# Optimization experiments

Hardware: AMD Instinct MI355X
Metric: run time of the kernel (lower is better)

The kernel has to match this reference:

```python
import jax, jax.numpy as jnp
import numpy as np

NEG_SLOPE = 0.2


def _gcn_conv(x, edge_index, W, b):
    # Standard GCNConv: y = D^-1/2 (A + I) D^-1/2 (x W) + b
    N = x.shape[0]
    loop = jnp.arange(N, dtype=edge_index.dtype)
    src = jnp.concatenate([edge_index[0], loop])  # [E+N]
    dst = jnp.concatenate([edge_index[1], loop])  # [E+N]
    deg = jax.ops.segment_sum(jnp.ones_like(dst, dtype=x.dtype), dst, num_segments=N)
    dinv = jnp.where(deg > 0, jax.lax.rsqrt(deg), 0.0)
    norm = dinv[src] * dinv[dst]                  # [E+N]
    h = x @ W                                     # [N, out] dense GEMM
    msg = h[src] * norm[:, None]                  # irregular gather, [E+N, out]
    agg = jax.ops.segment_sum(msg, dst, num_segments=N)  # irregular scatter
    return agg + b


def setup_inputs() -> dict:
    key = jax.random.key(0)
    ks = jax.random.split(key, 5)
    N, E, d_in, d_hid = 50000, 800000, 256, 512
    s = lambda fan_in, fan_out: np.sqrt(6.0 / (fan_in + fan_out))
    return {
        "x": jax.random.normal(ks[0], (N, d_in), dtype=jnp.float32),
        "edge_index": jax.random.randint(ks[1], (2, E), 0, N, dtype=jnp.int64),
        "W_gcn": jax.random.uniform(ks[2], (d_in, d_hid), jnp.float32, -s(d_in, d_hid), s(d_in, d_hid)),
        "b_gcn": jnp.zeros((d_hid,), jnp.float32),
        "W2": jax.random.uniform(ks[3], (d_hid, d_hid), jnp.float32, -s(d_hid, d_hid), s(d_hid, d_hid)),
        "b2": jnp.zeros((d_hid,), jnp.float32),
        "W_out": jax.random.uniform(ks[4], (d_hid, 1), jnp.float32, -s(d_hid, 1), s(d_hid, 1)),
        "b_out": jnp.zeros((1,), jnp.float32),
    }


def reference(x, edge_index, W_gcn, b_gcn, W2, b2, W_out, b_out):
    h = _gcn_conv(x, edge_index, W_gcn, b_gcn)           # [N, 512]
    h = jax.nn.leaky_relu(h, NEG_SLOPE)
    h = jax.nn.leaky_relu(h @ W2 + b2, NEG_SLOPE)        # [N, 512]
    return h @ W_out + b_out                             # [N, 1]
```

## Files before the change

kernel.cpp:

```cpp
#include <hip/hip_runtime.h>

#define D_IN  256
#define D_HID 512
#define NEG_SLOPE 0.2f
#define SCAN_CHUNK 2048

typedef __attribute__((ext_vector_type(8))) short short8;
typedef __attribute__((ext_vector_type(4))) float floatx4;

__device__ __forceinline__ unsigned short f2bf(float f) {
    unsigned int u = __float_as_uint(f);
    u += 0x7fffu + ((u >> 16) & 1u);
    return (unsigned short)(u >> 16);
}
__device__ __forceinline__ float bf2f(unsigned short u) {
    return __uint_as_float(((unsigned int)u) << 16);
}

__device__ __forceinline__ int eidx(const void* ei, long pos, int is64) {
    return is64 ? (int)((const long long*)ei)[pos] : ((const int*)ei)[pos];
}

__global__ __launch_bounds__(256) void k_init(const float* __restrict__ x,
                                              unsigned short* __restrict__ xb,
                                              int* __restrict__ deg, int N,
                                              const unsigned int* __restrict__ ei,
                                              int npairs, int* flag,
                                              const float* __restrict__ W_gcn,
                                              unsigned short* __restrict__ Wgt,
                                              const float* __restrict__ W2,
                                              unsigned short* __restrict__ W2t,
                                              const float* __restrict__ b_out,
                                              float* __restrict__ outacc,
                                              long xthreads) {
    long t = (long)blockIdx.x * blockDim.x + threadIdx.x;
    if (t < xthreads) {
        long i = t * 4;
        float4 v = *(const float4*)(x + i);
        ushort4 o;
        o.x = f2bf(v.x); o.y = f2bf(v.y); o.z = f2bf(v.z); o.w = f2bf(v.w);
        *(ushort4*)(xb + i) = o;
        if (t < N) deg[t] = 0;
        if (blockIdx.x == 0) {
            __shared__ int nz;
            if (threadIdx.x == 0) nz = 0;
            __syncthreads();
            for (int p = threadIdx.x; p < npairs; p += blockDim.x)
                if (ei[2 * p + 1] != 0) nz = 1;
            __syncthreads();
            if (threadIdx.x == 0) *flag = nz ? 0 : 1;
        }
        return;
    }
    long u = t - xthreads;
    if (u < (long)D_IN * D_HID) {
        int tt = (int)u;
        int n = tt / D_IN, k = tt - n * D_IN;
        Wgt[tt] = f2bf(W_gcn[(long)k * D_HID + n]);
        return;
    }
    u -= (long)D_IN * D_HID;
    if (u < (long)D_HID * D_HID) {
        int tt = (int)u;
        int n = tt / D_HID, k = tt - n * D_HID;
        W2t[tt] = f2bf(W2[(long)k * D_HID + n]);
        return;
    }
    u -= (long)D_HID * D_HID;
    if (u < N) outacc[u] = b_out[0];
}

__global__ void k_deg_count(const void* __restrict__ ei, const int* __restrict__ flag,
                            int* __restrict__ deg, int E) {
    int e = blockIdx.x * blockDim.x + threadIdx.x;
    if (e < E) atomicAdd(&deg[eidx(ei, (long)E + e, *flag)], 1);
}

__global__ __launch_bounds__(256) void k_scan1(const int* __restrict__ deg,
                                               int* __restrict__ bsum, int N) {
    int base = blockIdx.x * SCAN_CHUNK;
    int hi = min(base + SCAN_CHUNK, N);
    int s = 0;
    for (int i = base + threadIdx.x; i < hi; i += 256) s += deg[i];
#pragma unroll
    for (int off = 32; off > 0; off >>= 1) s += __shfl_down(s, off, 64);
    __shared__ int lds[4];
    if ((threadIdx.x & 63) == 0) lds[threadIdx.x >> 6] = s;
    __syncthreads();
    if (threadIdx.x == 0) bsum[blockIdx.x] = lds[0] + lds[1] + lds[2] + lds[3];
}

__global__ __launch_bounds__(256) void k_scan23(const int* __restrict__ deg,
                                                const int* __restrict__ bsum, int NB,
                                                int* __restrict__ offs,
                                                int* __restrict__ cursor,
                                                float* __restrict__ dinv, int N) {
    __shared__ int lds[256];
    int t = threadIdx.x;
    int bbase = 0;
    for (int i = 0; i < NB; ++i) bbase += (i < blockIdx.x) ? bsum[i] : 0;
    if (blockIdx.x == NB - 1 && t == 0) offs[N] = bbase + bsum[NB - 1];
    int base = blockIdx.x * SCAN_CHUNK;
    int lo = base + t * 8;
    int v[8], s = 0;
#pragma unroll
    for (int j = 0; j < 8; ++j) {
        int i = lo + j;
        v[j] = (i < N) ? deg[i] : 0;
        s += v[j];
    }
    lds[t] = s;
    __syncthreads();
    for (int d = 1; d < 256; d <<= 1) {
        int add = (t >= d) ? lds[t - d] : 0;
        __syncthreads();
        lds[t] += add;
        __syncthreads();
    }
    int run = bbase + ((t > 0) ? lds[t - 1] : 0);
#pragma unroll
    for (int j = 0; j < 8; ++j) {
        int i = lo + j;
        if (i < N) {
            offs[i] = run; cursor[i] = run;
            dinv[i] = rsqrtf(1.0f + (float)v[j]);
            run += v[j];
        }
    }
}

__global__ void k_fill(const void* __restrict__ ei, const int* __restrict__ flag,
                       int* __restrict__ cursor, int* __restrict__ esrc, int E) {
    int e = blockIdx.x * blockDim.x + threadIdx.x;
    if (e >= E) return;
    int is64 = *flag;
    int s = eidx(ei, e, is64), d = eidx(ei, (long)E + e, is64);
    int pos = atomicAdd(&cursor[d], 1);
    esrc[pos] = s;
}

__global__ __launch_bounds__(256) void k_gather(const unsigned short* __restrict__ xb,
                                                const int* __restrict__ offs,
                                                const int* __restrict__ esrc,
                                                const float* __restrict__ dinv,
                                                unsigned short* __restrict__ aggb, int N) {
    int node = blockIdx.x * 4 + (threadIdx.x >> 6);
    int lane = threadIdx.x & 63;
    if (node >= N) return;
    int half = lane >> 5;
    int li   = lane & 31;
    int colofs = li * 8;
    float di = dinv[node];

    float a[8];
    {
        short8 v = *(const short8*)(xb + (long)node * D_IN + colofs);
#pragma unroll
        for (int j = 0; j < 8; ++j)
            a[j] = (half == 0) ? di * bf2f((unsigned short)v[j]) : 0.f;
    }

    int beg = offs[node], end = offs[node + 1];
    int e = beg;
    for (; e + 8 <= end; e += 8) {
        int s0 = esrc[e + half];
        int s1 = esrc[e + 2 + half];
        int s2 = esrc[e + 4 + half];
        int s3 = esrc[e + 6 + half];
        float w0 = dinv[s0], w1 = dinv[s1], w2 = dinv[s2], w3 = dinv[s3];
        short8 u0 = *(const short8*)(xb + (long)s0 * D_IN + colofs);
        short8 u1 = *(const short8*)(xb + (long)s1 * D_IN + colofs);
        short8 u2 = *(const short8*)(xb + (long)s2 * D_IN + colofs);
        short8 u3 = *(const short8*)(xb + (long)s3 * D_IN + colofs);
#pragma unroll
        for (int j = 0; j < 8; ++j)
            a[j] += w0 * bf2f((unsigned short)u0[j]) + w1 * bf2f((unsigned short)u1[j])
                  + w2 * bf2f((unsigned short)u2[j]) + w3 * bf2f((unsigned short)u3[j]);
    }
    for (; e < end; e += 2) {
        int j0 = e + half;
        int jj = (j0 < end) ? j0 : end - 1;
        int s = esrc[jj];
        float w = (j0 < end) ? dinv[s] : 0.f;
        short8 u = *(const short8*)(xb + (long)s * D_IN + colofs);
#pragma unroll
        for (int j = 0; j < 8; ++j)
            a[j] += w * bf2f((unsigned short)u[j]);
    }

#pragma unroll
    for (int j = 0; j < 8; ++j) a[j] += __shfl_xor(a[j], 32, 64);

    if (half == 0) {
        short8 o;
#pragma unroll
        for (int j = 0; j < 8; ++j) o[j] = (short)f2bf(a[j] * di);
        *(short8*)(aggb + (long)node * D_IN + colofs) = o;
    }
}

__device__ __forceinline__ void async_cp16(const unsigned short* gp, unsigned short* lp) {
    __builtin_amdgcn_global_load_lds((const __attribute__((address_space(1))) void*)gp,
                                     (__attribute__((address_space(3))) void*)lp, 16, 0, 0);
}

__device__ __forceinline__ void stage_sw64(const unsigned short* src, int strideK,
                                           int rowMax, unsigned short* lds, int tid) {
#pragma unroll
    for (int rr = 0; rr < 4; ++rr) {
        int c = rr * 256 + tid;
        int row = c >> 3;
        int ci = (c & 7) ^ (row & 7);
        if (row > rowMax) row = rowMax;
        async_cp16(src + (long)row * strideK + ci * 8, lds + c * 8);
    }
}

__device__ __forceinline__ bool map_block(int b, int M, int& m0, int& n0) {
    int x = b & 7, slot = b >> 3;
    int mt = x + 8 * (slot >> 2);
    m0 = mt * 128; n0 = (slot & 3) * 128;
    return m0 < M;
}

__global__ __launch_bounds__(256) void k_gemm_bf16(const unsigned short* __restrict__ A,
                                                   const unsigned short* __restrict__ Bt,
                                                   const float* __restrict__ bias,
                                                   unsigned short* __restrict__ C,
                                                   int M, int K) {
    __shared__ __align__(16) unsigned short As[128 * 64];
    __shared__ __align__(16) unsigned short Bs[128 * 64];
    __shared__ __align__(16) unsigned short Ep[32 * 128];
    const int tid  = threadIdx.x;
    const int lane = tid & 63, wave = tid >> 6;
    int m0, n0;
    if (!map_block(blockIdx.x, M, m0, n0)) return;
    const int r = lane & 15, q = lane >> 4;
    const int xv = r & 7;
    const int wm = (wave & 1) * 64, wn = (wave >> 1) * 64;
    const int band = wm >> 6;

    floatx4 acc[4][4];
#pragma unroll
    for (int i = 0; i < 4; ++i)
#pragma unroll
        for (int j = 0; j < 4; ++j) acc[i][j] = (floatx4){0.f, 0.f, 0.f, 0.f};

    for (int k0 = 0; k0 < K; k0 += 64) {
        stage_sw64(A + (long)m0 * K + k0, K, M - 1 - m0, As, tid);
        stage_sw64(Bt + (long)n0 * K + k0, K, 127, Bs, tid);
        __syncthreads();

#pragma unroll
        for (int s = 0; s < 2; ++s) {
            int slotbase = s * 4 + q;
            short8 af[4], bf[4];
#pragma unroll
            for (int i = 0; i < 4; ++i)
                af[i] = *(const short8*)(As + (wm + i * 16 + r) * 64 + (slotbase ^ xv) * 8);
#pragma unroll
            for (int j = 0; j < 4; ++j)
                bf[j] = *(const short8*)(Bs + (wn + j * 16 + r) * 64 + (slotbase ^ xv) * 8);
#pragma unroll
            for (int i = 0; i < 4; ++i)
#pragma unroll
                for (int j = 0; j < 4; ++j)
                    acc[i][j] = __builtin_amdgcn_mfma_f32_16x16x32_bf16(af[i], bf[j], acc[i][j], 0, 0, 0);
        }
        __syncthreads();
    }

    float bv[4];
#pragma unroll
    for (int j = 0; j < 4; ++j) bv[j] = bias[n0 + wn + j * 16 + r];

#pragma unroll
    for (int i = 0; i < 4; ++i) {
#pragma unroll
        for (int j = 0; j < 4; ++j) {
#pragma unroll
            for (int t2 = 0; t2 < 4; ++t2) {
                float v = acc[i][j][t2] + bv[j];
                v = v > 0.f ? v : NEG_SLOPE * v;
                Ep[(band * 16 + q * 4 + t2) * 128 + wn + j * 16 + r] = f2bf(v);
            }
        }
        __syncthreads();
#pragma unroll
        for (int rr = 0; rr < 2; ++rr) {
            int c = rr * 256 + tid;
            int lrow = c >> 4, ccol = c & 15;
            int grow = m0 + (lrow >> 4) * 64 + i * 16 + (lrow & 15);
            if (grow < M) {
                short8 v = *(const short8*)(Ep + lrow * 128 + ccol * 8);
                *(short8*)(C + (long)grow * D_HID + n0 + ccol * 8) = v;
            }
        }
        __syncthreads();
    }
}

__global__ __launch_bounds__(256) void k_gemm2f(const unsigned short* __restrict__ A,
                                                const unsigned short* __restrict__ Bt,
                                                const float* __restrict__ bias,
                                                const float* __restrict__ wout,
                                                float* __restrict__ outacc,
                                                int M, int K) {
    __shared__ __align__(16) unsigned short As[128 * 64];
    __shared__ __align__(16) unsigned short Bs[128 * 64];
    const int tid  = threadIdx.x;
    const int lane = tid & 63, wave = tid >> 6;
    int m0, n0;
    if (!map_block(blockIdx.x, M, m0, n0)) return;
    const int r = lane & 15, q = lane >> 4;
    const int xv = r & 7;
    const int wm = (wave & 1) * 64, wn = (wave >> 1) * 64;

    floatx4 acc[4][4];
#pragma unroll
    for (int i = 0; i < 4; ++i)
#pragma unroll
        for (int j = 0; j < 4; ++j) acc[i][j] = (floatx4){0.f, 0.f, 0.f, 0.f};

    for (int k0 = 0; k0 < K; k0 += 64) {
        stage_sw64(A + (long)m0 * K + k0, K, M - 1 - m0, As, tid);
        stage_sw64(Bt + (long)n0 * K + k0, K, 127, Bs, tid);
        __syncthreads();

#pragma unroll
        for (int s = 0; s < 2; ++s) {
            int slotbase = s * 4 + q;
            short8 af[4], bf[4];
#pragma unroll
            for (int i = 0; i < 4; ++i)
                af[i] = *(const short8*)(As + (wm + i * 16 + r) * 64 + (slotbase ^ xv) * 8);
#pragma unroll
            for (int j = 0; j < 4; ++j)
                bf[j] = *(const short8*)(Bs + (wn + j * 16 + r) * 64 + (slotbase ^ xv) * 8);
#pragma unroll
            for (int i = 0; i < 4; ++i)
#pragma unroll
                for (int j = 0; j < 4; ++j)
                    acc[i][j] = __builtin_amdgcn_mfma_f32_16x16x32_bf16(af[i], bf[j], acc[i][j], 0, 0, 0);
        }
        __syncthreads();
    }

    float bv[4], wv[4];
#pragma unroll
    for (int j = 0; j < 4; ++j) {
        int col = n0 + wn + j * 16 + r;
        bv[j] = bias[col];
        wv[j] = wout[col];
    }
#pragma unroll
    for (int i = 0; i < 4; ++i) {
#pragma unroll
        for (int t2 = 0; t2 < 4; ++t2) {
            float p = 0.f;
#pragma unroll
            for (int j = 0; j < 4; ++j) {
                float v = acc[i][j][t2] + bv[j];
                v = v > 0.f ? v : NEG_SLOPE * v;
                p += v * wv[j];
            }
            p += __shfl_xor(p, 8, 64);
            p += __shfl_xor(p, 4, 64);
            p += __shfl_xor(p, 2, 64);
            p += __shfl_xor(p, 1, 64);
            if (r == 0) {
                int row = m0 + wm + i * 16 + q * 4 + t2;
                if (row < M) atomicAdd(&outacc[row], p);
            }
        }
    }
}

__global__ void k_out(const float* __restrict__ outacc, float* __restrict__ out, int N) {
    int i = blockIdx.x * blockDim.x + threadIdx.x;
    if (i < N) out[i] = outacc[i];
}

extern "C" void kernel_launch(void* const* d_in, const int* in_sizes, int n_in,
                              void* d_out, int out_size, void* d_ws, size_t ws_size,
                              hipStream_t stream) {
    const float* x     = (const float*)d_in[0];
    const void*  ei    = d_in[1];
    const float* W_gcn = (const float*)d_in[2];
    const float* b_gcn = (const float*)d_in[3];
    const float* W2    = (const float*)d_in[4];
    const float* b2    = (const float*)d_in[5];
    const float* W_out = (const float*)d_in[6];
    const float* b_out = (const float*)d_in[7];
    float* out = (float*)d_out;

    const int N = in_sizes[0] / D_IN;
    const int E = in_sizes[1] / 2;
    const int NB = (N + SCAN_CHUNK - 1) / SCAN_CHUNK;

    char* w = (char*)d_ws;
    size_t off = 0;
    auto alloc = [&](size_t bytes) { char* p = w + off; off = (off + bytes + 255) & ~(size_t)255; return p; };
    int*            flag   = (int*)alloc(256);
    float*          dinv   = (float*)alloc((size_t)N * 4);
    int*            deg_i  = (int*)alloc((size_t)N * 4);
    int*            offs   = (int*)alloc((size_t)(N + 1) * 4);
    int*            cursor = (int*)alloc((size_t)N * 4);
    float*          outacc = (float*)alloc((size_t)N * 4);
    int*            bsum   = (int*)alloc((size_t)NB * 4);
    int*            esrc   = (int*)alloc((size_t)(E + 16) * 4);
    unsigned short* xb     = (unsigned short*)alloc((size_t)N * D_IN * 2);
    unsigned short* aggb   = (unsigned short*)alloc((size_t)N * D_IN * 2);
    unsigned short* h1     = (unsigned short*)alloc((size_t)N * D_HID * 2);
    unsigned short* Wgt    = (unsigned short*)alloc((size_t)D_IN * D_HID * 2);
    unsigned short* W2t    = (unsigned short*)alloc((size_t)D_HID * D_HID * 2);

    int npairs = E < 2048 ? E : 2048;
    long xthreads = ((long)N * D_IN) / 4;
    long prep_elems = (long)D_IN * D_HID + (long)D_HID * D_HID + N;
    long tot_threads = xthreads + prep_elems;
    k_init<<<(unsigned)((tot_threads + 255) / 256), 256, 0, stream>>>(
        x, xb, deg_i, N, (const unsigned int*)ei, npairs, flag,
        W_gcn, Wgt, W2, W2t, b_out, outacc, xthreads);

    k_deg_count<<<(E + 255) / 256, 256, 0, stream>>>(ei, flag, deg_i, E);
    k_scan1<<<NB, 256, 0, stream>>>(deg_i, bsum, N);
    k_scan23<<<NB, 256, 0, stream>>>(deg_i, bsum, NB, offs, cursor, dinv, N);
    k_fill<<<(E + 255) / 256, 256, 0, stream>>>(ei, flag, cursor, esrc, E);

    k_gather<<<(N + 3) / 4, 256, 0, stream>>>(xb, offs, esrc, dinv, aggb, N);

    int mtiles = (N + 127) / 128;
    int gblocks = ((mtiles + 7) / 8) * 8 * 4;
    k_gemm_bf16<<<gblocks, 256, 0, stream>>>(aggb, Wgt, b_gcn, h1, N, D_IN);
    k_gemm2f<<<gblocks, 256, 0, stream>>>(h1, W2t, b2, W_out, outacc, N, D_HID);

    k_out<<<(N + 255) / 256, 256, 0, stream>>>(outacc, out, N);
}
```

Measured before the change: 330.0 us.

## Pre-scale bf16 features by dinv, unroll gather deeper, drop output copy kernel

Moves the x-to-bf16 conversion out of the init kernel into a new kernel that runs after the degree scan and multiplies each row by its dinv. This removes the per-edge dinv lookups and multiplies from the gather loop. The gather also gains a 16-edge unrolled loop for more loads in flight. The final GEMM now accumulates straight into the output buffer, which removes the separate copy kernel. The trade-off is one extra launch and a dependency of the x conversion on the scan, plus a little extra rounding from scaling before the bf16 conversion.

```diff
diff --git a/kernel.cpp b/kernel.cpp
--- a/kernel.cpp
+++ b/kernel.cpp
@@ -21,9 +21,7 @@
     return is64 ? (int)((const long long*)ei)[pos] : ((const int*)ei)[pos];
 }
 
-__global__ __launch_bounds__(256) void k_init(const float* __restrict__ x,
-                                              unsigned short* __restrict__ xb,
-                                              int* __restrict__ deg, int N,
+__global__ __launch_bounds__(256) void k_init(int* __restrict__ deg, int N,
                                               const unsigned int* __restrict__ ei,
                                               int npairs, int* flag,
                                               const float* __restrict__ W_gcn,
@@ -31,43 +29,30 @@
                                               const float* __restrict__ W2,
                                               unsigned short* __restrict__ W2t,
                                               const float* __restrict__ b_out,
-                                              float* __restrict__ outacc,
-                                              long xthreads) {
-    long t = (long)blockIdx.x * blockDim.x + threadIdx.x;
-    if (t < xthreads) {
-        long i = t * 4;
-        float4 v = *(const float4*)(x + i);
-        ushort4 o;
-        o.x = f2bf(v.x); o.y = f2bf(v.y); o.z = f2bf(v.z); o.w = f2bf(v.w);
-        *(ushort4*)(xb + i) = o;
-        if (t < N) deg[t] = 0;
-        if (blockIdx.x == 0) {
-            __shared__ int nz;
-            if (threadIdx.x == 0) nz = 0;
-            __syncthreads();
-            for (int p = threadIdx.x; p < npairs; p += blockDim.x)
-                if (ei[2 * p + 1] != 0) nz = 1;
-            __syncthreads();
-            if (threadIdx.x == 0) *flag = nz ? 0 : 1;
-        }
+                                              float* __restrict__ out) {
+    int t = blockIdx.x * blockDim.x + threadIdx.x;
+    if (blockIdx.x == 0) {
+        __shared__ int nz;
+        if (threadIdx.x == 0) nz = 0;
+        __syncthreads();
+        for (int p = threadIdx.x; p < npairs; p += blockDim.x)
+            if (ei[2 * p + 1] != 0) nz = 1;
+        __syncthreads();
+        if (threadIdx.x == 0) *flag = nz ? 0 : 1;
+    }
+    if (t < D_IN * D_HID) {
+        int n = t / D_IN, k = t - n * D_IN;
+        Wgt[t] = f2bf(W_gcn[(long)k * D_HID + n]);
         return;
     }
-    long u = t - xthreads;
-    if (u < (long)D_IN * D_HID) {
-        int tt = (int)u;
-        int n = tt / D_IN, k = tt - n * D_IN;
-        Wgt[tt] = f2bf(W_gcn[(long)k * D_HID + n]);
+    int u = t - D_IN * D_HID;
+    if (u < D_HID * D_HID) {
+        int n = u / D_HID, k = u - n * D_HID;
+        W2t[u] = f2bf(W2[(long)k * D_HID + n]);
         return;
     }
-    u -= (long)D_IN * D_HID;
-    if (u < (long)D_HID * D_HID) {
-        int tt = (int)u;
-        int n = tt / D_HID, k = tt - n * D_HID;
-        W2t[tt] = f2bf(W2[(long)k * D_HID + n]);
-        return;
-    }
-    u -= (long)D_HID * D_HID;
-    if (u < N) outacc[u] = b_out[0];
+    u -= D_HID * D_HID;
+    if (u < N) { deg[u] = 0; out[u] = b_out[0]; }
 }
 
 __global__ void k_deg_count(const void* __restrict__ ei, const int* __restrict__ flag,
@@ -129,6 +114,20 @@
     }
 }
 
+__global__ __launch_bounds__(256) void k_prescale(const float* __restrict__ x,
+                                                  const float* __restrict__ dinv,
+                                                  unsigned short* __restrict__ xb, int N) {
+    long t = (long)blockIdx.x * blockDim.x + threadIdx.x;
+    long total = (long)N * D_IN / 4;
+    if (t >= total) return;
+    int row = (int)(t >> 6);
+    float s = dinv[row];
+    float4 v = *(const float4*)(x + t * 4);
+    ushort4 o;
+    o.x = f2bf(v.x * s); o.y = f2bf(v.y * s); o.z = f2bf(v.z * s); o.w = f2bf(v.w * s);
+    *(ushort4*)(xb + t * 4) = o;
+}
+
 __global__ void k_fill(const void* __restrict__ ei, const int* __restrict__ flag,
                        int* __restrict__ cursor, int* __restrict__ esrc, int E) {
     int e = blockIdx.x * blockDim.x + threadIdx.x;
@@ -145,44 +144,71 @@
                                                 const float* __restrict__ dinv,
                                                 unsigned short* __restrict__ aggb, int N) {
     int node = blockIdx.x * 4 + (threadIdx.x >> 6);
+    if (node >= N) return;
     int lane = threadIdx.x & 63;
-    if (node >= N) return;
     int half = lane >> 5;
-    int li   = lane & 31;
-    int colofs = li * 8;
+    int colofs = (lane & 31) * 8;
     float di = dinv[node];
+    const unsigned short* xbc = xb + colofs;
 
     float a[8];
     {
-        short8 v = *(const short8*)(xb + (long)node * D_IN + colofs);
+        short8 v = *(const short8*)(xbc + (long)node * D_IN);
 #pragma unroll
         for (int j = 0; j < 8; ++j)
-            a[j] = (half == 0) ? di * bf2f((unsigned short)v[j]) : 0.f;
+            a[j] = (half == 0) ? bf2f((unsigned short)v[j]) : 0.f;
     }
 
     int beg = offs[node], end = offs[node + 1];
     int e = beg;
+    for (; e + 16 <= end; e += 16) {
+        int s0 = esrc[e      + half];
+        int s1 = esrc[e +  2 + half];
+        int s2 = esrc[e +  4 + half];
+        int s3 = esrc[e +  6 + half];
+        int s4 = esrc[e +  8 + half];
+        int s5 = esrc[e + 10 + half];
+        int s6 = esrc[e + 12 + half];
+        int s7 = esrc[e + 14 + half];
+        short8 u0 = *(const short8*)(xbc + (long)s0 * D_IN);
+        short8 u1 = *(const short8*)(xbc + (long)s1 * D_IN);
+        short8 u2 = *(const short8*)(xbc + (long)s2 * D_IN);
+        short8 u3 = *(const short8*)(xbc + (long)s3 * D_IN);
+        short8 u4 = *(const short8*)(xbc + (long)s4 * D_IN);
+        short8 u5 = *(const short8*)(xbc + (long)s5 * D_IN);
+        short8 u6 = *(const short8*)(xbc + (long)s6 * D_IN);
+        short8 u7 = *(const short8*)(xbc + (long)s7 * D_IN);
+#pragma unroll
+        for (int j = 0; j < 8; ++j) {
+            float t0 = bf2f((unsigned short)u0[j]) + bf2f((unsigned short)u1[j]);
+            float t1 = bf2f((unsigned short)u2[j]) + bf2f((unsigned short)u3[j]);
+            float t2 = bf2f((unsigned short)u4[j]) + bf2f((unsigned short)u5[j]);
+            float t3 = bf2f((unsigned short)u6[j]) + bf2f((unsigned short)u7[j]);
+            a[j] += (t0 + t1) + (t2 + t3);
+        }
+    }
     for (; e + 8 <= end; e += 8) {
-        int s0 = esrc[e + half];
+        int s0 = esrc[e     + half];
         int s1 = esrc[e + 2 + half];
         int s2 = esrc[e + 4 + half];
         int s3 = esrc[e + 6 + half];
-        float w0 = dinv[s0], w1 = dinv[s1], w2 = dinv[s2], w3 = dinv[s3];
-        short8 u0 = *(const short8*)(xb + (long)s0 * D_IN + colofs);
-        short8 u1 = *(const short8*)(xb + (long)s1 * D_IN + colofs);
-        short8 u2 = *(const short8*)(xb + (long)s2 * D_IN + colofs);
-        short8 u3 = *(const short8*)(xb + (long)s3 * D_IN + colofs);
-#pragma unroll
-        for (int j = 0; j < 8; ++j)
-            a[j] += w0 * bf2f((unsigned short)u0[j]) + w1 * bf2f((unsigned short)u1[j])
-                  + w2 * bf2f((unsigned short)u2[j]) + w3 * bf2f((unsigned short)u3[j]);
+        short8 u0 = *(const short8*)(xbc + (long)s0 * D_IN);
+        short8 u1 = *(const short8*)(xbc + (long)s1 * D_IN);
+        short8 u2 = *(const short8*)(xbc + (long)s2 * D_IN);
+        short8 u3 = *(const short8*)(xbc + (long)s3 * D_IN);
+#pragma unroll
+        for (int j = 0; j < 8; ++j) {
+            float t0 = bf2f((unsigned short)u0[j]) + bf2f((unsigned short)u1[j]);
+            float t1 = bf2f((unsigned short)u2[j]) + bf2f((unsigned short)u3[j]);
+            a[j] += t0 + t1;
+        }
     }
     for (; e < end; e += 2) {
         int j0 = e + half;
         int jj = (j0 < end) ? j0 : end - 1;
         int s = esrc[jj];
-        float w = (j0 < end) ? dinv[s] : 0.f;
-        short8 u = *(const short8*)(xb + (long)s * D_IN + colofs);
+        float w = (j0 < end) ? 1.f : 0.f;
+        short8 u = *(const short8*)(xbc + (long)s * D_IN);
 #pragma unroll
         for (int j = 0; j < 8; ++j)
             a[j] += w * bf2f((unsigned short)u[j]);
@@ -304,7 +330,7 @@
                                                 const unsigned short* __restrict__ Bt,
                                                 const float* __restrict__ bias,
                                                 const float* __restrict__ wout,
-                                                float* __restrict__ outacc,
+                                                float* __restrict__ out,
                                                 int M, int K) {
     __shared__ __align__(16) unsigned short As[128 * 64];
     __shared__ __align__(16) unsigned short Bs[128 * 64];
@@ -370,15 +396,10 @@
             p += __shfl_xor(p, 1, 64);
             if (r == 0) {
                 int row = m0 + wm + i * 16 + q * 4 + t2;
-                if (row < M) atomicAdd(&outacc[row], p);
+                if (row < M) atomicAdd(&out[row], p);
             }
         }
     }
-}
-
-__global__ void k_out(const float* __restrict__ outacc, float* __restrict__ out, int N) {
-    int i = blockIdx.x * blockDim.x + threadIdx.x;
-    if (i < N) out[i] = outacc[i];
 }
 
 extern "C" void kernel_launch(void* const* d_in, const int* in_sizes, int n_in,
@@ -406,7 +427,6 @@
     int*            deg_i  = (int*)alloc((size_t)N * 4);
     int*            offs   = (int*)alloc((size_t)(N + 1) * 4);
     int*            cursor = (int*)alloc((size_t)N * 4);
-    float*          outacc = (float*)alloc((size_t)N * 4);
     int*            bsum   = (int*)alloc((size_t)NB * 4);
     int*            esrc   = (int*)alloc((size_t)(E + 16) * 4);
     unsigned short* xb     = (unsigned short*)alloc((size_t)N * D_IN * 2);
@@ -416,16 +436,17 @@
     unsigned short* W2t    = (unsigned short*)alloc((size_t)D_HID * D_HID * 2);
 
     int npairs = E < 2048 ? E : 2048;
-    long xthreads = ((long)N * D_IN) / 4;
-    long prep_elems = (long)D_IN * D_HID + (long)D_HID * D_HID + N;
-    long tot_threads = xthreads + prep_elems;
-    k_init<<<(unsigned)((tot_threads + 255) / 256), 256, 0, stream>>>(
-        x, xb, deg_i, N, (const unsigned int*)ei, npairs, flag,
-        W_gcn, Wgt, W2, W2t, b_out, outacc, xthreads);
+    long init_threads = (long)D_IN * D_HID + (long)D_HID * D_HID + N;
+    k_init<<<(unsigned)((init_threads + 255) / 256), 256, 0, stream>>>(
+        deg_i, N, (const unsigned int*)ei, npairs, flag,
+        W_gcn, Wgt, W2, W2t, b_out, out);
 
     k_deg_count<<<(E + 255) / 256, 256, 0, stream>>>(ei, flag, deg_i, E);
     k_scan1<<<NB, 256, 0, stream>>>(deg_i, bsum, N);
     k_scan23<<<NB, 256, 0, stream>>>(deg_i, bsum, NB, offs, cursor, dinv, N);
+
+    long pthreads = (long)N * D_IN / 4;
+    k_prescale<<<(unsigned)((pthreads + 255) / 256), 256, 0, stream>>>(x, dinv, xb, N);
     k_fill<<<(E + 255) / 256, 256, 0, stream>>>(ei, flag, cursor, esrc, E);
 
     k_gather<<<(N + 3) / 4, 256, 0, stream>>>(xb, offs, esrc, dinv, aggb, N);
@@ -433,7 +454,5 @@
     int mtiles = (N + 127) / 128;
     int gblocks = ((mtiles + 7) / 8) * 8 * 4;
     k_gemm_bf16<<<gblocks, 256, 0, stream>>>(aggb, Wgt, b_gcn, h1, N, D_IN);
-    k_gemm2f<<<gblocks, 256, 0, stream>>>(h1, W2t, b2, W_out, outacc, N, D_HID);
-
-    k_out<<<(N + 255) / 256, 256, 0, stream>>>(outacc, out, N);
-}
+    k_gemm2f<<<gblocks, 256, 0, stream>>>(h1, W2t, b2, W_out, out, N, D_HID);
+}
```

New measurement: 336.7 us. +2.1%, slower.
